# Performance work log

Hardware: AMD Instinct MI355X
Metric: run time of the kernel (lower is better)

Reference implementation:

```python
import jax, jax.numpy as jnp
import numpy as np

N_WIRES = 5
BATCH = 262144
TWO_PI = 2.0 * np.pi

H = (jnp.array([[1.0, 1.0], [1.0, -1.0]], dtype=jnp.complex64) / np.sqrt(2.0).astype(np.float32))
X = jnp.array([[0.0, 1.0], [1.0, 0.0]], dtype=jnp.complex64)


def rz(phi):
    # RZ(phi) = diag(e^{-i phi/2}, e^{+i phi/2})
    em = jnp.exp(-0.5j * phi)
    ep = jnp.exp(0.5j * phi)
    zero = jnp.zeros_like(em)
    return jnp.stack([jnp.stack([em, zero]), jnp.stack([zero, ep])])


def s_gate(z):
    # RX(-2*acos(z)) = [[z, i*sqrt(1-z^2)], [i*sqrt(1-z^2), z]]
    c = z.astype(jnp.complex64)
    s = 1j * jnp.sqrt(1.0 - z * z).astype(jnp.complex64)
    return jnp.stack([jnp.stack([c, s]), jnp.stack([s, c])])


def apply_gate(psi, U, target, controls=()):
    # psi: (2,)*N_WIRES complex state; apply 2x2 U on `target`, conditioned on
    # all `controls` being |1>. Static indices -> jit/vmap friendly.
    idx = tuple(1 if w in controls else slice(None) for w in range(N_WIRES))
    sub = psi[idx]
    t_ax = target - sum(c < target for c in controls)
    sub = jnp.moveaxis(jnp.tensordot(U, sub, axes=([1], [t_ax])), 0, t_ax)
    return psi.at[idx].set(sub)


def u_qsp(psi, phases, z, wire, controls):
    # RZ(ph[0]) then repeat (S(z), RZ(ph[k])) -- phases length is static
    psi = apply_gate(psi, rz(phases[0]), wire, controls)
    Sz = s_gate(z)
    for k in range(1, phases.shape[0]):
        psi = apply_gate(psi, Sz, wire, controls)
        psi = apply_gate(psi, rz(phases[k]), wire, controls)
    return psi


def f_single(t, x, ph_x1, ph_x2, ph_t1, ph_t2):
    psi = jnp.zeros((2,) * N_WIRES, dtype=jnp.complex64).at[(0,) * N_WIRES].set(1.0)
    for w in range(N_WIRES):
        psi = apply_gate(psi, H, w)
    # ctrl(W_lcu, control=0): every inner gate gains control wire 0
    psi = apply_gate(psi, X, 1, controls=(0,))
    psi = u_qsp(psi, ph_x1, x, 2, controls=(0, 1))
    psi = apply_gate(psi, X, 1, controls=(0,))
    psi = u_qsp(psi, ph_x2, x, 2, controls=(0, 1))
    psi = apply_gate(psi, X, 3, controls=(0,))
    psi = u_qsp(psi, ph_t1, t, 4, controls=(0, 3))
    psi = apply_gate(psi, X, 3, controls=(0,))
    psi = u_qsp(psi, ph_t2, t, 4, controls=(0, 3))
    psi = apply_gate(psi, H, 0)
    probs = psi.real ** 2 + psi.imag ** 2  # (2,)*5
    return probs[0].sum() - probs[1].sum()  # <Z_0>


def setup_inputs() -> dict:
    key = jax.random.key(0)
    k_t, k_x, k1, k2, k3, k4 = jax.random.split(key, 6)
    return {
        "t": jax.random.uniform(k_t, (BATCH, 1), dtype=jnp.float32),
        "x": jax.random.uniform(k_x, (BATCH, 1), dtype=jnp.float32),
        "ph_x1": TWO_PI * jax.random.uniform(k1, (3,), dtype=jnp.float32),
        "ph_x2": TWO_PI * jax.random.uniform(k2, (4,), dtype=jnp.float32),
        "ph_t1": TWO_PI * jax.random.uniform(k3, (3,), dtype=jnp.float32),
        "ph_t2": TWO_PI * jax.random.uniform(k4, (4,), dtype=jnp.float32),
    }


def reference(t, x, ph_x1, ph_x2, ph_t1, ph_t2):
    out = jax.vmap(f_single, in_axes=(0, 0, None, None, None, None))(
        t[:, 0], x[:, 0], ph_x1, ph_x2, ph_t1, ph_t2
    )
    return out[:, None]  # (batch, 1)
```

## Files before the change

### kernel.cpp

```cpp
#include <hip/hip_runtime.h>
#include <math.h>


__device__ __forceinline__ float2 cmul(float2 a, float2 b) {
    return make_float2(fmaf(a.x, b.x, -a.y * b.y), fmaf(a.x, b.y, a.y * b.x));
}

template <int N>
__device__ __forceinline__ float2 qsp_A(const float* c, const float* s,
                                        float z, float sz) {
    float2 m00 = make_float2(c[0], -s[0]);
    float2 m01 = make_float2(0.f, 0.f);
    float2 m10 = make_float2(0.f, 0.f);
    float2 m11 = make_float2(c[0],  s[0]);
#pragma unroll
    for (int k = 1; k < N; ++k) {
        float2 n00 = make_float2(z * m00.x - sz * m10.y, z * m00.y + sz * m10.x);
        float2 n01 = make_float2(z * m01.x - sz * m11.y, z * m01.y + sz * m11.x);
        float2 n10 = make_float2(z * m10.x - sz * m00.y, z * m10.y + sz * m00.x);
        float2 n11 = make_float2(z * m11.x - sz * m01.y, z * m11.y + sz * m01.x);
        float2 e0 = make_float2(c[k], -s[k]);
        float2 e1 = make_float2(c[k],  s[k]);
        m00 = cmul(e0, n00); m01 = cmul(e0, n01);
        m10 = cmul(e1, n10); m11 = cmul(e1, n11);
    }
    return make_float2(0.5f * (m00.x + m01.x + m10.x + m11.x),
                       0.5f * (m00.y + m01.y + m10.y + m11.y));
}

struct Phases {
    float cx1[3], sx1[3], cx2[4], sx2[4];
    float ct1[3], st1[3], ct2[4], st2[4];
};

__device__ __forceinline__ float f_one(float tt, float xx, const Phases& P) {
    float sx = sqrtf(fmaxf(0.f, 1.f - xx * xx));
    float st = sqrtf(fmaxf(0.f, 1.f - tt * tt));
    float2 Ax1 = qsp_A<3>(P.cx1, P.sx1, xx, sx);
    float2 Ax2 = qsp_A<4>(P.cx2, P.sx2, xx, sx);
    float2 At1 = qsp_A<3>(P.ct1, P.st1, tt, st);
    float2 At2 = qsp_A<4>(P.ct2, P.st2, tt, st);
    float2 Ax = make_float2(Ax1.x + Ax2.x, Ax1.y + Ax2.y);
    float2 At = make_float2(At1.x + At2.x, At1.y + At2.y);
    return 0.25f * (Ax.x * At.x - Ax.y * At.y);
}

__global__ __launch_bounds__(256) void qpinn_kernel(
    const float* __restrict__ t, const float* __restrict__ x,
    const float* __restrict__ phx1, const float* __restrict__ phx2,
    const float* __restrict__ pht1, const float* __restrict__ pht2,
    float* __restrict__ out, int n) {
    int i = blockIdx.x * blockDim.x + threadIdx.x;

    Phases P;
#pragma unroll
    for (int k = 0; k < 3; ++k) sincosf(0.5f * phx1[k], &P.sx1[k], &P.cx1[k]);
#pragma unroll
    for (int k = 0; k < 4; ++k) sincosf(0.5f * phx2[k], &P.sx2[k], &P.cx2[k]);
#pragma unroll
    for (int k = 0; k < 3; ++k) sincosf(0.5f * pht1[k], &P.st1[k], &P.ct1[k]);
#pragma unroll
    for (int k = 0; k < 4; ++k) sincosf(0.5f * pht2[k], &P.st2[k], &P.ct2[k]);

    int base = i * 4;
    if (base + 3 < n) {
        float4 tv = *reinterpret_cast<const float4*>(t + base);
        float4 xv = *reinterpret_cast<const float4*>(x + base);
        float4 ov;
        ov.x = f_one(tv.x, xv.x, P);
        ov.y = f_one(tv.y, xv.y, P);
        ov.z = f_one(tv.z, xv.z, P);
        ov.w = f_one(tv.w, xv.w, P);
        *reinterpret_cast<float4*>(out + base) = ov;
    } else {
        for (int j = base; j < n; ++j) out[j] = f_one(t[j], x[j], P);
    }
}

extern "C" void kernel_launch(void* const* d_in, const int* in_sizes, int n_in,
                              void* d_out, int out_size, void* d_ws, size_t ws_size,
                              hipStream_t stream) {
    const float* t    = (const float*)d_in[0];
    const float* x    = (const float*)d_in[1];
    const float* phx1 = (const float*)d_in[2];
    const float* phx2 = (const float*)d_in[3];
    const float* pht1 = (const float*)d_in[4];
    const float* pht2 = (const float*)d_in[5];
    float* out = (float*)d_out;
    int n = out_size;
    int groups = (n + 3) / 4;
    int block = 256;
    int grid = (groups + block - 1) / block;
    qpinn_kernel<<<grid, block, 0, stream>>>(t, x, phx1, phx2, pht1, pht2, out, n);
}
```

Before: 11.29 us.

## Compute phase sincos once per block in shared memory; process two elements per thread

Moves the 14 phase sincos evaluations from every thread into the first 14 threads of each block. The results go to shared memory, followed by a block barrier. Each thread now handles two batch elements with float2 loads instead of four with float4, which doubles the thread count. This removes redundant transcendental work per thread at the cost of a __syncthreads, shared-memory reads and narrower vector memory accesses.

```diff
diff --git a/kernel.cpp b/kernel.cpp
--- a/kernel.cpp
+++ b/kernel.cpp
@@ -50,30 +50,41 @@
     const float* __restrict__ phx1, const float* __restrict__ phx2,
     const float* __restrict__ pht1, const float* __restrict__ pht2,
     float* __restrict__ out, int n) {
-    int i = blockIdx.x * blockDim.x + threadIdx.x;
+    __shared__ float sc[14], cc[14];
+    int tid = threadIdx.x;
+    if (tid < 14) {
+        float p;
+        if (tid < 3)       p = phx1[tid];
+        else if (tid < 7)  p = phx2[tid - 3];
+        else if (tid < 10) p = pht1[tid - 7];
+        else               p = pht2[tid - 10];
+        float s, c;
+        sincosf(0.5f * p, &s, &c);
+        sc[tid] = s; cc[tid] = c;
+    }
+    __syncthreads();
 
     Phases P;
 #pragma unroll
-    for (int k = 0; k < 3; ++k) sincosf(0.5f * phx1[k], &P.sx1[k], &P.cx1[k]);
+    for (int k = 0; k < 3; ++k) { P.sx1[k] = sc[k];      P.cx1[k] = cc[k]; }
 #pragma unroll
-    for (int k = 0; k < 4; ++k) sincosf(0.5f * phx2[k], &P.sx2[k], &P.cx2[k]);
+    for (int k = 0; k < 4; ++k) { P.sx2[k] = sc[3 + k];  P.cx2[k] = cc[3 + k]; }
 #pragma unroll
-    for (int k = 0; k < 3; ++k) sincosf(0.5f * pht1[k], &P.st1[k], &P.ct1[k]);
+    for (int k = 0; k < 3; ++k) { P.st1[k] = sc[7 + k];  P.ct1[k] = cc[7 + k]; }
 #pragma unroll
-    for (int k = 0; k < 4; ++k) sincosf(0.5f * pht2[k], &P.st2[k], &P.ct2[k]);
+    for (int k = 0; k < 4; ++k) { P.st2[k] = sc[10 + k]; P.ct2[k] = cc[10 + k]; }
 
-    int base = i * 4;
-    if (base + 3 < n) {
-        float4 tv = *reinterpret_cast<const float4*>(t + base);
-        float4 xv = *reinterpret_cast<const float4*>(x + base);
-        float4 ov;
+    int i = blockIdx.x * blockDim.x + tid;
+    int base = i * 2;
+    if (base + 1 < n) {
+        float2 tv = *reinterpret_cast<const float2*>(t + base);
+        float2 xv = *reinterpret_cast<const float2*>(x + base);
+        float2 ov;
         ov.x = f_one(tv.x, xv.x, P);
         ov.y = f_one(tv.y, xv.y, P);
-        ov.z = f_one(tv.z, xv.z, P);
-        ov.w = f_one(tv.w, xv.w, P);
-        *reinterpret_cast<float4*>(out + base) = ov;
-    } else {
-        for (int j = base; j < n; ++j) out[j] = f_one(t[j], x[j], P);
+        *reinterpret_cast<float2*>(out + base) = ov;
+    } else if (base < n) {
+        out[base] = f_one(t[base], x[base], P);
     }
 }
 
@@ -88,7 +99,7 @@
     const float* pht2 = (const float*)d_in[5];
     float* out = (float*)d_out;
     int n = out_size;
-    int groups = (n + 3) / 4;
+    int groups = (n + 1) / 2;
     int block = 256;
     int grid = (groups + block - 1) / block;
     qpinn_kernel<<<grid, block, 0, stream>>>(t, x, phx1, phx2, pht1, pht2, out, n);
```

Measured after the change: 17.25 us. +52.8%, slower.
